# Performance work log

Measured on AMD Instinct MI355X. Metric: run time of the kernel, lower is better.

## Reference

```python
import jax, jax.numpy as jnp
import numpy as np

N_HEADS = 16
N_KV_HEADS = 4
HEAD_DIM = 128
NEG_INF = -1e9


def setup_inputs() -> dict:
    key = jax.random.key(0)
    ks = jax.random.split(key, 6)
    bs, seq, d_model = 2, 2048, 2048
    x = jax.random.normal(ks[0], (bs, seq, d_model), jnp.float32)
    # RoPE table: theta = 10000^{-2i/head_dim}, angle = pos * theta
    inv_freq = 1.0 / (10000.0 ** (jnp.arange(0, HEAD_DIM, 2, dtype=jnp.float32) / HEAD_DIM))
    ang = jnp.arange(seq, dtype=jnp.float32)[:, None] * inv_freq[None, :]  # [seq, head_dim/2]
    freqs_cos = jnp.cos(ang)
    freqs_sin = jnp.sin(ang)
    # causal additive mask
    mask = jnp.where(jnp.tril(jnp.ones((seq, seq), dtype=bool)), 0.0, NEG_INF).astype(jnp.float32)
    s = 1.0 / np.sqrt(d_model)
    wq = jax.random.normal(ks[1], (d_model, N_HEADS * HEAD_DIM), jnp.float32) * s
    wk = jax.random.normal(ks[2], (d_model, N_KV_HEADS * HEAD_DIM), jnp.float32) * s
    wv = jax.random.normal(ks[3], (d_model, N_KV_HEADS * HEAD_DIM), jnp.float32) * s
    wo = jax.random.normal(ks[4], (N_HEADS * HEAD_DIM, d_model), jnp.float32) * s
    return {"x": x, "freqs_cos": freqs_cos, "freqs_sin": freqs_sin, "mask": mask,
            "wq": wq, "wk": wk, "wv": wv, "wo": wo}


def _rope(t, cos, sin):
    # t: [b, h, s, d]; cos/sin: [s, d/2]
    b, h, s, d = t.shape
    tp = t.reshape(b, h, s, d // 2, 2)
    x0, x1 = tp[..., 0], tp[..., 1]
    c = cos[None, None, :, :]
    sn = sin[None, None, :, :]
    o0 = x0 * c - x1 * sn
    o1 = x0 * sn + x1 * c
    return jnp.stack([o0, o1], axis=-1).reshape(b, h, s, d)


def reference(x, freqs_cos, freqs_sin, mask, wq, wk, wv, wo):
    bs, seq, d_model = x.shape
    rep = N_HEADS // N_KV_HEADS
    q = (x @ wq).reshape(bs, seq, N_HEADS, HEAD_DIM).transpose(0, 2, 1, 3)
    k = (x @ wk).reshape(bs, seq, N_KV_HEADS, HEAD_DIM).transpose(0, 2, 1, 3)
    v = (x @ wv).reshape(bs, seq, N_KV_HEADS, HEAD_DIM).transpose(0, 2, 1, 3)
    q = _rope(q, freqs_cos, freqs_sin)
    k = _rope(k, freqs_cos, freqs_sin)
    # GQA: group q heads over kv heads instead of materially repeating kv
    qg = q.reshape(bs, N_KV_HEADS, rep, seq, HEAD_DIM)
    scores = jnp.einsum('bgrsd,bgtd->bgrst', qg, k) / np.sqrt(HEAD_DIM)
    scores = scores + mask[None, None, None, :, :]
    attn = jax.nn.softmax(scores, axis=-1)
    out = jnp.einsum('bgrst,bgtd->bgrsd', attn, v)
    out = out.reshape(bs, N_HEADS, seq, HEAD_DIM).transpose(0, 2, 1, 3).reshape(bs, seq, -1)
    return out @ wo
```

## Files before the change

kernel.cpp:

```cpp
#include <hip/hip_runtime.h>
#include <hip/hip_bf16.h>

#define SEQ 2048
#define DM 2048
#define NH 16
#define NKV 4
#define HD 128

typedef float f32x4 __attribute__((ext_vector_type(4)));
typedef short s16x8 __attribute__((ext_vector_type(8)));
typedef short s16x4 __attribute__((ext_vector_type(4)));

__device__ inline __hip_bfloat16 f2b(float f) { return __float2bfloat16(f); }
__device__ inline float b2f_us(unsigned short u) { return __uint_as_float(((unsigned)u) << 16); }
__device__ inline short f2b_s(float f) {
    __hip_bfloat16 h = __float2bfloat16(f);
    return *(short*)&h;
}

__device__ inline void gl_lds16(const void* g, void* l) {
    __builtin_amdgcn_global_load_lds((const __attribute__((address_space(1))) void*)g,
                                     (__attribute__((address_space(3))) void*)l, 16, 0, 0);
}

__global__ void prep_kernel(const float* __restrict__ x,
                            const float* __restrict__ wq, const float* __restrict__ wk,
                            const float* __restrict__ wv, const float* __restrict__ wo,
                            __hip_bfloat16* __restrict__ xb,
                            __hip_bfloat16* __restrict__ wqkvt,
                            __hip_bfloat16* __restrict__ wot) {
    __shared__ float tile[32][33];
    int bid = blockIdx.x;
    const int t = threadIdx.x;
    if (bid < 8192) {
        int i = (bid * 256 + t) * 4;
        float4 v = *(const float4*)(x + i);
        __hip_bfloat16 o4[4] = {f2b(v.x), f2b(v.y), f2b(v.z), f2b(v.w)};
        *(ushort4*)(xb + i) = *(ushort4*)o4;
        return;
    }
    bid -= 8192;
    const float* in;
    __hip_bfloat16* out;
    int N, bx, by;
    if (bid < 4096) {
        in = wq; out = wqkvt; N = 2048; bx = bid & 63; by = bid >> 6;
    } else if (bid < 5120) {
        bid -= 4096; in = wk; out = wqkvt + (size_t)2048 * 2048; N = 512; bx = bid & 15; by = bid >> 4;
    } else if (bid < 6144) {
        bid -= 5120; in = wv; out = wqkvt + (size_t)2560 * 2048; N = 512; bx = bid & 15; by = bid >> 4;
    } else {
        bid -= 6144; in = wo; out = wot; N = 2048; bx = bid & 63; by = bid >> 6;
    }
    const int K = 2048;
    int n0 = bx * 32, k0 = by * 32;
    int tx = t & 31, ty = t >> 5;
    for (int r = ty; r < 32; r += 8)
        tile[r][tx] = in[(size_t)(k0 + r) * N + n0 + tx];
    __syncthreads();
    for (int r = ty; r < 32; r += 8)
        out[(size_t)(n0 + r) * K + k0 + tx] = f2b(tile[tx][r]);
}

template <int OUT_F32>
__global__ __launch_bounds__(256, 3) void gemm_bt(
    const __hip_bfloat16* __restrict__ A,
    const __hip_bfloat16* __restrict__ Bt,
    void* __restrict__ Cp, int M, int N, int Kd) {
    __shared__ __hip_bfloat16 As[128 * 64];
    __shared__ __hip_bfloat16 Bs[128 * 64];
    const int nx = gridDim.x, ny = gridDim.y;
    const int pid = blockIdx.y * nx + blockIdx.x;
    const int GM = 8;
    const int grp = pid / (GM * nx);
    const int first = grp * GM;
    const int gsz = (ny - first < GM) ? (ny - first) : GM;
    const int mt = first + (pid % gsz);
    const int ntile = (pid % (GM * nx)) / gsz;
    const int m0 = mt * 128, n0 = ntile * 128;

    const int t = threadIdx.x;
    const int wv = t >> 6, lane = t & 63;
    const int wm = (wv >> 1) * 64, wn = (wv & 1) * 64;
    const int lrow = lane & 15, quad = lane >> 4;
    f32x4 acc[4][4];
    f32x4 z4 = {0.f, 0.f, 0.f, 0.f};
    for (int i = 0; i < 4; ++i)
        for (int j = 0; j < 4; ++j) acc[i][j] = z4;

    for (int k0 = 0; k0 < Kd; k0 += 64) {
        __syncthreads();
        for (int i = 0; i < 4; ++i) {
            int flat = i * 256 + t;
            int row = flat >> 3;
            int cb = (flat & 7) ^ (row & 7);
            gl_lds16(A + (size_t)(m0 + row) * Kd + k0 + cb * 8, &As[flat * 8]);
            gl_lds16(Bt + (size_t)(n0 + row) * Kd + k0 + cb * 8, &Bs[flat * 8]);
        }
        __syncthreads();
        for (int kk = 0; kk < 2; ++kk) {
            s16x8 af[4], bf[4];
            for (int i = 0; i < 4; ++i) {
                int ra = wm + i * 16 + lrow;
                int rb = wn + i * 16 + lrow;
                int pba = ((kk * 4 + quad) ^ (ra & 7)) * 8;
                int pbb = ((kk * 4 + quad) ^ (rb & 7)) * 8;
                af[i] = *(const s16x8*)&As[ra * 64 + pba];
                bf[i] = *(const s16x8*)&Bs[rb * 64 + pbb];
            }
            for (int i = 0; i < 4; ++i)
                for (int j = 0; j < 4; ++j)
                    acc[i][j] = __builtin_amdgcn_mfma_f32_16x16x32_bf16(af[i], bf[j],
                                                                        acc[i][j], 0, 0, 0);
        }
    }
    for (int i = 0; i < 4; ++i)
        for (int j = 0; j < 4; ++j)
            for (int r = 0; r < 4; ++r) {
                int m = m0 + wm + i * 16 + quad * 4 + r;
                int n = n0 + wn + j * 16 + lrow;
                if (OUT_F32)
                    ((float*)Cp)[(size_t)m * N + n] = acc[i][j][r];
                else
                    ((__hip_bfloat16*)Cp)[(size_t)m * N + n] = f2b(acc[i][j][r]);
            }
}

#define QSC 0.12751744f
__global__ void rv_kernel(const __hip_bfloat16* __restrict__ qkv,
                          const float* __restrict__ fcos, const float* __restrict__ fsin,
                          __hip_bfloat16* __restrict__ q, __hip_bfloat16* __restrict__ k,
                          __hip_bfloat16* __restrict__ vt) {
    __shared__ __hip_bfloat16 tile[128][136];
    const int t = threadIdx.x;
    if (blockIdx.x < 4096) {
        int tok = blockIdx.x;
        int b = tok >> 11, s = tok & 2047;
        const __hip_bfloat16* row = qkv + (size_t)tok * 3072;
        for (int it = t; it < 320; it += 256) {
            int col = it * 8;
            s16x8 v = *(const s16x8*)(row + col);
            int p0 = (col & 127) >> 1;
            f32x4 c4 = *(const f32x4*)(fcos + s * 64 + p0);
            f32x4 s4 = *(const f32x4*)(fsin + s * 64 + p0);
            float scl = (col < 2048) ? QSC : 1.0f;
            short outv[8];
            for (int p = 0; p < 4; ++p) {
                float x0 = b2f_us((unsigned short)v[2 * p]);
                float x1 = b2f_us((unsigned short)v[2 * p + 1]);
                outv[2 * p] = f2b_s((x0 * c4[p] - x1 * s4[p]) * scl);
                outv[2 * p + 1] = f2b_s((x0 * s4[p] + x1 * c4[p]) * scl);
            }
            int d = col & 127;
            if (col < 2048) {
                int h = col >> 7;
                *(s16x8*)(q + ((size_t)((b * NH + h) * SEQ + s)) * HD + d) = *(s16x8*)outv;
            } else {
                int h = (col - 2048) >> 7;
                *(s16x8*)(k + ((size_t)((b * NKV + h) * SEQ + s)) * HD + d) = *(s16x8*)outv;
            }
        }
        return;
    }
    int r = blockIdx.x - 4096;
    int s0 = (r & 15) * 128;
    int bh = r >> 4;
    int b = bh >> 2, kvh = bh & 3;
    for (int i = 0; i < 8; ++i) {
        int flat = (i * 256 + t) * 8;
        int row = flat >> 7, col = flat & 127;
        *(s16x8*)&tile[row][col] =
            *(const s16x8*)(qkv + (size_t)(b * SEQ + s0 + row) * 3072 + 2560 + kvh * 128 + col);
    }
    __syncthreads();
    for (int i = 0; i < 8; ++i) {
        int dd = i * 16 + (t >> 4);
        int ss = (t & 15) * 8;
        __hip_bfloat16 tmp[8];
        for (int j = 0; j < 8; ++j) tmp[j] = tile[ss + j][dd];
        *(s16x8*)(vt + ((size_t)((b * NKV + kvh) * HD + dd)) * SEQ + s0 + ss) = *(s16x8*)tmp;
    }
}

__global__ __launch_bounds__(512, 4) void attn_kernel(
    const __hip_bfloat16* __restrict__ q, const __hip_bfloat16* __restrict__ k,
    const __hip_bfloat16* __restrict__ vt, __hip_bfloat16* __restrict__ o) {
    __shared__ __hip_bfloat16 Ks[64][136];
    __shared__ __hip_bfloat16 Vs[128][72];

    const int bh = blockIdx.y;
    const int bx = (bh < 16) ? (int)(gridDim.x - 1 - blockIdx.x) : (int)blockIdx.x;
    const int b = bh >> 4, h = bh & 15;
    const int kvh = h >> 2;
    const int t = threadIdx.x;
    const int w = t >> 6, lane = t & 63;
    const int lrow = lane & 15, quad = lane >> 4;
    const int q0 = bx * 128;
    const int qrow = q0 + w * 16 + lrow;

    const __hip_bfloat16* qp = q + ((size_t)((b * NH + h) * SEQ + qrow)) * HD;
    s16x8 qf[4];
    for (int ks = 0; ks < 4; ++ks) qf[ks] = *(const s16x8*)(qp + ks * 32 + quad * 8);

    float m_i = -1e30f, l_i = 0.f;
    f32x4 accO[8];
    f32x4 z4 = {0.f, 0.f, 0.f, 0.f};
    for (int d = 0; d < 8; ++d) accO[d] = z4;

    const __hip_bfloat16* kbase = k + ((size_t)(b * NKV + kvh) * SEQ) * HD;
    const __hip_bfloat16* vbase = vt + ((size_t)(b * NKV + kvh) * HD) * SEQ;

    s16x8 kr[2], vr[2];
    auto load_tile = [&](int kt) {
        for (int i = 0; i < 2; ++i) {
            int flat = (i * 512 + t) * 8;
            kr[i] = *(const s16x8*)(kbase + (size_t)(kt * 64 + (flat >> 7)) * HD + (flat & 127));
            vr[i] = *(const s16x8*)(vbase + (size_t)(flat >> 6) * SEQ + kt * 64 + (flat & 63));
        }
    };
    auto store_tile = [&]() {
        for (int i = 0; i < 2; ++i) {
            int flat = (i * 512 + t) * 8;
            *(s16x8*)&Ks[flat >> 7][flat & 127] = kr[i];
            int row = flat >> 6, k0 = flat & 63;
            int pb = ((k0 >> 5) << 5) | (((k0 >> 2) & 2) << 3) | (((k0 >> 4) & 1) << 2);
            s16x4 lo = {vr[i][0], vr[i][1], vr[i][2], vr[i][3]};
            s16x4 hi = {vr[i][4], vr[i][5], vr[i][6], vr[i][7]};
            *(s16x4*)&Vs[row][pb] = lo;
            *(s16x4*)&Vs[row][pb + 8] = hi;
        }
    };

    const int nkt = 2 * bx + 2;
    load_tile(0);
    store_tile();

    for (int kt = 0; kt < nkt; ++kt) {
        bool more = (kt + 1) < nkt;
        __syncthreads();
        if (more) load_tile(kt + 1);
        bool wave_active = (kt * 64 <= q0 + w * 16 + 15);
        bool mtile = (kt >= 2 * bx);

        if (wave_active) {
            float sv[4][4];
            __builtin_amdgcn_s_setprio(1);
            for (int nt = 0; nt < 4; ++nt) {
                f32x4 sacc = z4;
                for (int ks = 0; ks < 4; ++ks) {
                    s16x8 kf = *(const s16x8*)&Ks[nt * 16 + lrow][ks * 32 + quad * 8];
                    sacc = __builtin_amdgcn_mfma_f32_16x16x32_bf16(kf, qf[ks], sacc, 0, 0, 0);
                }
                if (mtile) {
                    for (int r = 0; r < 4; ++r) {
                        int key = kt * 64 + nt * 16 + quad * 4 + r;
                        sv[nt][r] = (key > qrow) ? -1e30f : sacc[r];
                    }
                } else {
                    for (int r = 0; r < 4; ++r) sv[nt][r] = sacc[r];
                }
            }
            __builtin_amdgcn_s_setprio(0);
            float mt2 = fmaxf(fmaxf(fmaxf(sv[0][0], sv[0][1]), fmaxf(sv[0][2], sv[0][3])),
                              fmaxf(fmaxf(sv[1][0], sv[1][1]), fmaxf(sv[1][2], sv[1][3])));
            mt2 = fmaxf(mt2,
                        fmaxf(fmaxf(fmaxf(sv[2][0], sv[2][1]), fmaxf(sv[2][2], sv[2][3])),
                              fmaxf(fmaxf(sv[3][0], sv[3][1]), fmaxf(sv[3][2], sv[3][3]))));
            mt2 = fmaxf(mt2, __shfl_xor(mt2, 16, 64));
            mt2 = fmaxf(mt2, __shfl_xor(mt2, 32, 64));
            if (!__all(mt2 <= m_i + 8.f)) {
                float mn = fmaxf(m_i, mt2);
                float alpha = exp2f(m_i - mn);
                l_i *= alpha;
                for (int d = 0; d < 8; ++d)
                    for (int r = 0; r < 4; ++r) accO[d][r] *= alpha;
                m_i = mn;
            }
            float rs = 0.f;
            s16x8 pf0, pf1;
#pragma unroll
            for (int j = 0; j < 8; ++j) {
                float p0 = exp2f(sv[j >> 2][j & 3] - m_i);
                float p1 = exp2f(sv[2 + (j >> 2)][j & 3] - m_i);
                rs += p0 + p1;
                pf0[j] = f2b_s(p0);
                pf1[j] = f2b_s(p1);
            }
            rs += __shfl_xor(rs, 16, 64);
            rs += __shfl_xor(rs, 32, 64);
            l_i += rs;
            __builtin_amdgcn_s_setprio(1);
            for (int dt = 0; dt < 8; ++dt) {
                s16x8 vf0 = *(const s16x8*)&Vs[dt * 16 + lrow][quad * 8];
                s16x8 vf1 = *(const s16x8*)&Vs[dt * 16 + lrow][32 + quad * 8];
                accO[dt] = __builtin_amdgcn_mfma_f32_16x16x32_bf16(vf0, pf0, accO[dt], 0, 0, 0);
                accO[dt] = __builtin_amdgcn_mfma_f32_16x16x32_bf16(vf1, pf1, accO[dt], 0, 0, 0);
            }
            __builtin_amdgcn_s_setprio(0);
        }

        __syncthreads();
        if (more) store_tile();
    }
    float inv = 1.0f / l_i;
    __hip_bfloat16* op = o + (size_t)(b * SEQ + qrow) * DM + h * HD;
    for (int dt = 0; dt < 8; ++dt) {
        short ov[4];
        for (int r = 0; r < 4; ++r) ov[r] = f2b_s(accO[dt][r] * inv);
        *(s16x4*)(op + dt * 16 + quad * 4) = *(s16x4*)ov;
    }
}

extern "C" void kernel_launch(void* const* d_in, const int* in_sizes, int n_in,
                              void* d_out, int out_size, void* d_ws, size_t ws_size,
                              hipStream_t stream) {
    (void)in_sizes; (void)n_in; (void)out_size; (void)ws_size;
    const float* x  = (const float*)d_in[0];
    const float* fc = (const float*)d_in[1];
    const float* fs = (const float*)d_in[2];
    const float* wq = (const float*)d_in[4];
    const float* wk = (const float*)d_in[5];
    const float* wv = (const float*)d_in[6];
    const float* wo = (const float*)d_in[7];

    __hip_bfloat16* xb    = (__hip_bfloat16*)d_ws;
    __hip_bfloat16* wqkvt = xb + (size_t)8388608;
    __hip_bfloat16* wot   = wqkvt + (size_t)6291456;
    __hip_bfloat16* qkv   = wot + (size_t)4194304;
    __hip_bfloat16* qb    = xb;
    __hip_bfloat16* kb    = wqkvt;
    __hip_bfloat16* vtb   = wqkvt + (size_t)2097152;
    __hip_bfloat16* attno = qkv;

    prep_kernel<<<18432, 256, 0, stream>>>(x, wq, wk, wv, wo, xb, wqkvt, wot);
    gemm_bt<0><<<dim3(24, 32), 256, 0, stream>>>(xb, wqkvt, qkv, 4096, 3072, 2048);
    rv_kernel<<<4224, 256, 0, stream>>>(qkv, fc, fs, qb, kb, vtb);
    attn_kernel<<<dim3(16, 32), 512, 0, stream>>>(qb, kb, vtb, attno);
    gemm_bt<1><<<dim3(16, 32), 256, 0, stream>>>(attno, wot, d_out, 4096, 2048, 2048);
}
```

Baseline: 331.1 us.

## Switch attention kernel to 32x32x16 MFMA with 4 waves of 32 query rows

Rewrites the attention inner loop to use 32x32x16 bf16 MFMA instead of 16x16x32, with each of 4 waves handling 32 query rows (256 threads per block instead of 512). The P matrix is repacked from the S accumulator layout into B-operand layout using v_permlane32_swap, removing the permuted V store layout in LDS. This is meant to cut LDS reads per FLOP and instruction overhead, but it raises register pressure (larger accumulators, 8 Q fragments) and lowers the wave count per block.

```diff
diff --git a/kernel.cpp b/kernel.cpp
--- a/kernel.cpp
+++ b/kernel.cpp
@@ -8,14 +8,24 @@
 #define HD 128
 
 typedef float f32x4 __attribute__((ext_vector_type(4)));
+typedef float f32x16 __attribute__((ext_vector_type(16)));
 typedef short s16x8 __attribute__((ext_vector_type(8)));
 typedef short s16x4 __attribute__((ext_vector_type(4)));
+typedef unsigned u32x4 __attribute__((ext_vector_type(4)));
 
 __device__ inline __hip_bfloat16 f2b(float f) { return __float2bfloat16(f); }
 __device__ inline float b2f_us(unsigned short u) { return __uint_as_float(((unsigned)u) << 16); }
 __device__ inline short f2b_s(float f) {
     __hip_bfloat16 h = __float2bfloat16(f);
     return *(short*)&h;
+}
+__device__ inline unsigned pk2(float lo, float hi) {
+    unsigned a = (unsigned)(unsigned short)f2b_s(lo);
+    unsigned b = (unsigned)(unsigned short)f2b_s(hi);
+    return a | (b << 16);
+}
+__device__ inline void pl32swap(unsigned& a, unsigned& b) {
+    asm("v_permlane32_swap_b32 %0, %1" : "+v"(a), "+v"(b));
 }
 
 __device__ inline void gl_lds16(const void* g, void* l) {
@@ -182,7 +192,7 @@
     }
 }
 
-__global__ __launch_bounds__(512, 4) void attn_kernel(
+__global__ __launch_bounds__(256, 2) void attn_kernel(
     const __hip_bfloat16* __restrict__ q, const __hip_bfloat16* __restrict__ k,
     const __hip_bfloat16* __restrict__ vt, __hip_bfloat16* __restrict__ o) {
     __shared__ __hip_bfloat16 Ks[64][136];
@@ -190,44 +200,44 @@
 
     const int bh = blockIdx.y;
     const int bx = (bh < 16) ? (int)(gridDim.x - 1 - blockIdx.x) : (int)blockIdx.x;
-    const int b = bh >> 4, h = bh & 15;
-    const int kvh = h >> 2;
+    const int b = bh >> 4, hh = bh & 15;
+    const int kvh = hh >> 2;
     const int t = threadIdx.x;
     const int w = t >> 6, lane = t & 63;
-    const int lrow = lane & 15, quad = lane >> 4;
+    const int l31 = lane & 31, hf = lane >> 5;
     const int q0 = bx * 128;
-    const int qrow = q0 + w * 16 + lrow;
-
-    const __hip_bfloat16* qp = q + ((size_t)((b * NH + h) * SEQ + qrow)) * HD;
-    s16x8 qf[4];
-    for (int ks = 0; ks < 4; ++ks) qf[ks] = *(const s16x8*)(qp + ks * 32 + quad * 8);
+    const int qrow = q0 + w * 32 + l31;
+
+    const __hip_bfloat16* qp = q + ((size_t)((b * NH + hh) * SEQ + qrow)) * HD;
+    s16x8 qf[8];
+#pragma unroll
+    for (int kw = 0; kw < 8; ++kw) qf[kw] = *(const s16x8*)(qp + kw * 16 + hf * 8);
 
     float m_i = -1e30f, l_i = 0.f;
-    f32x4 accO[8];
-    f32x4 z4 = {0.f, 0.f, 0.f, 0.f};
-    for (int d = 0; d < 8; ++d) accO[d] = z4;
+    f32x16 accO[4];
+#pragma unroll
+    for (int db = 0; db < 4; ++db)
+#pragma unroll
+        for (int r = 0; r < 16; ++r) accO[db][r] = 0.f;
 
     const __hip_bfloat16* kbase = k + ((size_t)(b * NKV + kvh) * SEQ) * HD;
     const __hip_bfloat16* vbase = vt + ((size_t)(b * NKV + kvh) * HD) * SEQ;
 
-    s16x8 kr[2], vr[2];
+    s16x8 kr[4], vr[4];
     auto load_tile = [&](int kt) {
-        for (int i = 0; i < 2; ++i) {
-            int flat = (i * 512 + t) * 8;
+#pragma unroll
+        for (int i = 0; i < 4; ++i) {
+            int flat = (i * 256 + t) * 8;
             kr[i] = *(const s16x8*)(kbase + (size_t)(kt * 64 + (flat >> 7)) * HD + (flat & 127));
             vr[i] = *(const s16x8*)(vbase + (size_t)(flat >> 6) * SEQ + kt * 64 + (flat & 63));
         }
     };
     auto store_tile = [&]() {
-        for (int i = 0; i < 2; ++i) {
-            int flat = (i * 512 + t) * 8;
+#pragma unroll
+        for (int i = 0; i < 4; ++i) {
+            int flat = (i * 256 + t) * 8;
             *(s16x8*)&Ks[flat >> 7][flat & 127] = kr[i];
-            int row = flat >> 6, k0 = flat & 63;
-            int pb = ((k0 >> 5) << 5) | (((k0 >> 2) & 2) << 3) | (((k0 >> 4) & 1) << 2);
-            s16x4 lo = {vr[i][0], vr[i][1], vr[i][2], vr[i][3]};
-            s16x4 hi = {vr[i][4], vr[i][5], vr[i][6], vr[i][7]};
-            *(s16x4*)&Vs[row][pb] = lo;
-            *(s16x4*)&Vs[row][pb + 8] = hi;
+            *(s16x8*)&Vs[flat >> 6][flat & 63] = vr[i];
         }
     };
 
@@ -239,62 +249,85 @@
         bool more = (kt + 1) < nkt;
         __syncthreads();
         if (more) load_tile(kt + 1);
-        bool wave_active = (kt * 64 <= q0 + w * 16 + 15);
+        bool wave_active = (kt * 64 <= q0 + w * 32 + 31);
         bool mtile = (kt >= 2 * bx);
 
         if (wave_active) {
-            float sv[4][4];
+            f32x16 s0, s1;
+#pragma unroll
+            for (int r = 0; r < 16; ++r) { s0[r] = 0.f; s1[r] = 0.f; }
             __builtin_amdgcn_s_setprio(1);
-            for (int nt = 0; nt < 4; ++nt) {
-                f32x4 sacc = z4;
-                for (int ks = 0; ks < 4; ++ks) {
-                    s16x8 kf = *(const s16x8*)&Ks[nt * 16 + lrow][ks * 32 + quad * 8];
-                    sacc = __builtin_amdgcn_mfma_f32_16x16x32_bf16(kf, qf[ks], sacc, 0, 0, 0);
+#pragma unroll
+            for (int kw = 0; kw < 8; ++kw) {
+                s16x8 kf0 = *(const s16x8*)&Ks[l31][kw * 16 + hf * 8];
+                s16x8 kf1 = *(const s16x8*)&Ks[32 + l31][kw * 16 + hf * 8];
+                s0 = __builtin_amdgcn_mfma_f32_32x32x16_bf16(kf0, qf[kw], s0, 0, 0, 0);
+                s1 = __builtin_amdgcn_mfma_f32_32x32x16_bf16(kf1, qf[kw], s1, 0, 0, 0);
+            }
+            __builtin_amdgcn_s_setprio(0);
+            if (mtile) {
+#pragma unroll
+                for (int r = 0; r < 16; ++r) {
+                    int key0 = kt * 64 + (r & 3) + 8 * (r >> 2) + 4 * hf;
+                    if (key0 > qrow) s0[r] = -1e30f;
+                    if (key0 + 32 > qrow) s1[r] = -1e30f;
                 }
-                if (mtile) {
-                    for (int r = 0; r < 4; ++r) {
-                        int key = kt * 64 + nt * 16 + quad * 4 + r;
-                        sv[nt][r] = (key > qrow) ? -1e30f : sacc[r];
-                    }
-                } else {
-                    for (int r = 0; r < 4; ++r) sv[nt][r] = sacc[r];
-                }
-            }
-            __builtin_amdgcn_s_setprio(0);
-            float mt2 = fmaxf(fmaxf(fmaxf(sv[0][0], sv[0][1]), fmaxf(sv[0][2], sv[0][3])),
-                              fmaxf(fmaxf(sv[1][0], sv[1][1]), fmaxf(sv[1][2], sv[1][3])));
-            mt2 = fmaxf(mt2,
-                        fmaxf(fmaxf(fmaxf(sv[2][0], sv[2][1]), fmaxf(sv[2][2], sv[2][3])),
-                              fmaxf(fmaxf(sv[3][0], sv[3][1]), fmaxf(sv[3][2], sv[3][3]))));
-            mt2 = fmaxf(mt2, __shfl_xor(mt2, 16, 64));
+            }
+            float mt2 = -1e30f;
+#pragma unroll
+            for (int r = 0; r < 16; ++r) mt2 = fmaxf(mt2, fmaxf(s0[r], s1[r]));
             mt2 = fmaxf(mt2, __shfl_xor(mt2, 32, 64));
             if (!__all(mt2 <= m_i + 8.f)) {
                 float mn = fmaxf(m_i, mt2);
                 float alpha = exp2f(m_i - mn);
                 l_i *= alpha;
-                for (int d = 0; d < 8; ++d)
-                    for (int r = 0; r < 4; ++r) accO[d][r] *= alpha;
+#pragma unroll
+                for (int db = 0; db < 4; ++db)
+#pragma unroll
+                    for (int r = 0; r < 16; ++r) accO[db][r] *= alpha;
                 m_i = mn;
             }
             float rs = 0.f;
-            s16x8 pf0, pf1;
-#pragma unroll
-            for (int j = 0; j < 8; ++j) {
-                float p0 = exp2f(sv[j >> 2][j & 3] - m_i);
-                float p1 = exp2f(sv[2 + (j >> 2)][j & 3] - m_i);
-                rs += p0 + p1;
-                pf0[j] = f2b_s(p0);
-                pf1[j] = f2b_s(p1);
-            }
-            rs += __shfl_xor(rs, 16, 64);
+            unsigned c[16];
+#pragma unroll
+            for (int r = 0; r < 8; ++r) {
+                float pa = exp2f(s0[2 * r] - m_i);
+                float pb = exp2f(s0[2 * r + 1] - m_i);
+                rs += pa + pb;
+                c[r] = pk2(pa, pb);
+            }
+#pragma unroll
+            for (int r = 0; r < 8; ++r) {
+                float pa = exp2f(s1[2 * r] - m_i);
+                float pb = exp2f(s1[2 * r + 1] - m_i);
+                rs += pa + pb;
+                c[8 + r] = pk2(pa, pb);
+            }
             rs += __shfl_xor(rs, 32, 64);
             l_i += rs;
+            pl32swap(c[0], c[2]);  pl32swap(c[1], c[3]);
+            pl32swap(c[4], c[6]);  pl32swap(c[5], c[7]);
+            pl32swap(c[8], c[10]); pl32swap(c[9], c[11]);
+            pl32swap(c[12], c[14]); pl32swap(c[13], c[15]);
+            u32x4 pw0 = {c[0], c[1], c[2], c[3]};
+            u32x4 pw1 = {c[4], c[5], c[6], c[7]};
+            u32x4 pw2 = {c[8], c[9], c[10], c[11]};
+            u32x4 pw3 = {c[12], c[13], c[14], c[15]};
+            s16x8 pf0 = __builtin_bit_cast(s16x8, pw0);
+            s16x8 pf1 = __builtin_bit_cast(s16x8, pw1);
+            s16x8 pf2 = __builtin_bit_cast(s16x8, pw2);
+            s16x8 pf3 = __builtin_bit_cast(s16x8, pw3);
             __builtin_amdgcn_s_setprio(1);
-            for (int dt = 0; dt < 8; ++dt) {
-                s16x8 vf0 = *(const s16x8*)&Vs[dt * 16 + lrow][quad * 8];
-                s16x8 vf1 = *(const s16x8*)&Vs[dt * 16 + lrow][32 + quad * 8];
-                accO[dt] = __builtin_amdgcn_mfma_f32_16x16x32_bf16(vf0, pf0, accO[dt], 0, 0, 0);
-                accO[dt] = __builtin_amdgcn_mfma_f32_16x16x32_bf16(vf1, pf1, accO[dt], 0, 0, 0);
+#pragma unroll
+            for (int db = 0; db < 4; ++db) {
+                s16x8 vf0 = *(const s16x8*)&Vs[db * 32 + l31][0 + hf * 8];
+                s16x8 vf1 = *(const s16x8*)&Vs[db * 32 + l31][16 + hf * 8];
+                s16x8 vf2 = *(const s16x8*)&Vs[db * 32 + l31][32 + hf * 8];
+                s16x8 vf3 = *(const s16x8*)&Vs[db * 32 + l31][48 + hf * 8];
+                accO[db] = __builtin_amdgcn_mfma_f32_32x32x16_bf16(vf0, pf0, accO[db], 0, 0, 0);
+                accO[db] = __builtin_amdgcn_mfma_f32_32x32x16_bf16(vf1, pf1, accO[db], 0, 0, 0);
+                accO[db] = __builtin_amdgcn_mfma_f32_32x32x16_bf16(vf2, pf2, accO[db], 0, 0, 0);
+                accO[db] = __builtin_amdgcn_mfma_f32_32x32x16_bf16(vf3, pf3, accO[db], 0, 0, 0);
             }
             __builtin_amdgcn_s_setprio(0);
         }
@@ -303,12 +336,16 @@
         if (more) store_tile();
     }
     float inv = 1.0f / l_i;
-    __hip_bfloat16* op = o + (size_t)(b * SEQ + qrow) * DM + h * HD;
-    for (int dt = 0; dt < 8; ++dt) {
-        short ov[4];
-        for (int r = 0; r < 4; ++r) ov[r] = f2b_s(accO[dt][r] * inv);
-        *(s16x4*)(op + dt * 16 + quad * 4) = *(s16x4*)ov;
-    }
+    __hip_bfloat16* op = o + (size_t)(b * SEQ + qrow) * DM + hh * HD;
+#pragma unroll
+    for (int db = 0; db < 4; ++db)
+#pragma unroll
+        for (int g = 0; g < 4; ++g) {
+            short ov[4];
+#pragma unroll
+            for (int e = 0; e < 4; ++e) ov[e] = f2b_s(accO[db][4 * g + e] * inv);
+            *(s16x4*)(op + db * 32 + g * 8 + hf * 4) = *(s16x4*)ov;
+        }
 }
 
 extern "C" void kernel_launch(void* const* d_in, const int* in_sizes, int n_in,
@@ -335,6 +372,6 @@
     prep_kernel<<<18432, 256, 0, stream>>>(x, wq, wk, wv, wo, xb, wqkvt, wot);
     gemm_bt<0><<<dim3(24, 32), 256, 0, stream>>>(xb, wqkvt, qkv, 4096, 3072, 2048);
     rv_kernel<<<4224, 256, 0, stream>>>(qkv, fc, fs, qb, kb, vtb);
-    attn_kernel<<<dim3(16, 32), 512, 0, stream>>>(qb, kb, vtb, attno);
+    attn_kernel<<<dim3(16, 32), 256, 0, stream>>>(qb, kb, vtb, attno);
     gemm_bt<1><<<dim3(16, 32), 256, 0, stream>>>(attno, wot, d_out, 4096, 2048, 2048);
 }
```

After: 343.9 us. 1.04x slower.

## Split attention KV range across two wave groups with LDS merge

Applied to the files above, without the earlier changes.

Each block now handles 64 query rows instead of 128, and the grid doubles. The eight waves form two halves that walk disjoint halves of the causal KV range (32-key tiles), each keeping its own online-softmax state. At the end the two partial results are merged through LDS. K tiles are loaded directly into LDS with global_load_lds and an XOR swizzle instead of going through registers. This targets causal load imbalance and the per-block serial KV loop length, at the cost of more blocks, smaller MFMA tiles per step, and an extra merge pass.

```diff
diff --git a/kernel.cpp b/kernel.cpp
--- a/kernel.cpp
+++ b/kernel.cpp
@@ -185,8 +185,12 @@
 __global__ __launch_bounds__(512, 4) void attn_kernel(
     const __hip_bfloat16* __restrict__ q, const __hip_bfloat16* __restrict__ k,
     const __hip_bfloat16* __restrict__ vt, __hip_bfloat16* __restrict__ o) {
-    __shared__ __hip_bfloat16 Ks[64][136];
-    __shared__ __hip_bfloat16 Vs[128][72];
+    __shared__ __attribute__((aligned(16))) char smem[34816];
+    __hip_bfloat16* KsA = (__hip_bfloat16*)smem;
+    __hip_bfloat16* KsB = KsA + 32 * 128;
+    __hip_bfloat16* VsA = KsB + 32 * 128;
+    __hip_bfloat16* VsB = VsA + 128 * 36;
+    float* mrg = (float*)smem;
 
     const int bh = blockIdx.y;
     const int bx = (bh < 16) ? (int)(gridDim.x - 1 - blockIdx.x) : (int)blockIdx.x;
@@ -194,9 +198,11 @@
     const int kvh = h >> 2;
     const int t = threadIdx.x;
     const int w = t >> 6, lane = t & 63;
+    const int g = w & 3, half = w >> 2;
     const int lrow = lane & 15, quad = lane >> 4;
-    const int q0 = bx * 128;
-    const int qrow = q0 + w * 16 + lrow;
+    const int q0 = bx * 64;
+    const int qrow = q0 + g * 16 + lrow;
+    const int Tg = 2 * bx + 1 + (g >> 1);
 
     const __hip_bfloat16* qp = q + ((size_t)((b * NH + h) * SEQ + qrow)) * HD;
     s16x8 qf[4];
@@ -210,50 +216,58 @@
     const __hip_bfloat16* kbase = k + ((size_t)(b * NKV + kvh) * SEQ) * HD;
     const __hip_bfloat16* vbase = vt + ((size_t)(b * NKV + kvh) * HD) * SEQ;
 
-    s16x8 kr[2], vr[2];
-    auto load_tile = [&](int kt) {
-        for (int i = 0; i < 2; ++i) {
-            int flat = (i * 512 + t) * 8;
-            kr[i] = *(const s16x8*)(kbase + (size_t)(kt * 64 + (flat >> 7)) * HD + (flat & 127));
-            vr[i] = *(const s16x8*)(vbase + (size_t)(flat >> 6) * SEQ + kt * 64 + (flat & 63));
-        }
+    auto issue_k = [&](int kt, __hip_bfloat16* dst) {
+        const __hip_bfloat16* src = kbase + (size_t)(kt * 32 + (t >> 4)) * HD +
+                                    (((t & 15) ^ ((t >> 4) & 7)) << 3);
+        gl_lds16(src, dst + t * 8);
     };
-    auto store_tile = [&]() {
-        for (int i = 0; i < 2; ++i) {
-            int flat = (i * 512 + t) * 8;
-            *(s16x8*)&Ks[flat >> 7][flat & 127] = kr[i];
-            int row = flat >> 6, k0 = flat & 63;
-            int pb = ((k0 >> 5) << 5) | (((k0 >> 2) & 2) << 3) | (((k0 >> 4) & 1) << 2);
-            s16x4 lo = {vr[i][0], vr[i][1], vr[i][2], vr[i][3]};
-            s16x4 hi = {vr[i][4], vr[i][5], vr[i][6], vr[i][7]};
-            *(s16x4*)&Vs[row][pb] = lo;
-            *(s16x4*)&Vs[row][pb + 8] = hi;
-        }
+    s16x8 vr[2];
+    auto load_v = [&](int ka, int kb) {
+        int row = t >> 2, k0 = (t & 3) * 8;
+        vr[0] = *(const s16x8*)(vbase + (size_t)row * SEQ + ka * 32 + k0);
+        vr[1] = *(const s16x8*)(vbase + (size_t)row * SEQ + kb * 32 + k0);
     };
-
-    const int nkt = 2 * bx + 2;
-    load_tile(0);
-    store_tile();
-
-    for (int kt = 0; kt < nkt; ++kt) {
-        bool more = (kt + 1) < nkt;
+    auto store_v = [&]() {
+        int row = t >> 2, k0 = (t & 3) * 8;
+        int pb = (((k0 >> 2) & 3) << 3) | (((k0 >> 4) & 1) << 2);
+        s16x4 lo0 = {vr[0][0], vr[0][1], vr[0][2], vr[0][3]};
+        s16x4 hi0 = {vr[0][4], vr[0][5], vr[0][6], vr[0][7]};
+        s16x4 lo1 = {vr[1][0], vr[1][1], vr[1][2], vr[1][3]};
+        s16x4 hi1 = {vr[1][4], vr[1][5], vr[1][6], vr[1][7]};
+        *(s16x4*)&VsA[row * 36 + pb] = lo0;
+        *(s16x4*)&VsA[row * 36 + pb + 8] = hi0;
+        *(s16x4*)&VsB[row * 36 + pb] = lo1;
+        *(s16x4*)&VsB[row * 36 + pb + 8] = hi1;
+    };
+
+    issue_k(0, KsA);
+    issue_k(bx + 1, KsB);
+    load_v(0, bx + 1);
+    store_v();
+
+    for (int s = 0; s <= bx; ++s) {
         __syncthreads();
-        if (more) load_tile(kt + 1);
-        bool wave_active = (kt * 64 <= q0 + w * 16 + 15);
-        bool mtile = (kt >= 2 * bx);
-
-        if (wave_active) {
-            float sv[4][4];
+        const bool more = s < bx;
+        if (more) load_v(s + 1, bx + s + 2);
+
+        const int kt = half ? (bx + 1 + s) : s;
+        const bool active = half ? (bx + 1 + s < Tg) : true;
+        if (active) {
+            const __hip_bfloat16* Ksm = half ? KsB : KsA;
+            const __hip_bfloat16* Vsm = half ? VsB : VsA;
+            const bool mtile = (kt * 32 + 31 > q0 + g * 16);
+            float sv[2][4];
             __builtin_amdgcn_s_setprio(1);
-            for (int nt = 0; nt < 4; ++nt) {
+            for (int nt = 0; nt < 2; ++nt) {
                 f32x4 sacc = z4;
                 for (int ks = 0; ks < 4; ++ks) {
-                    s16x8 kf = *(const s16x8*)&Ks[nt * 16 + lrow][ks * 32 + quad * 8];
+                    s16x8 kf = *(const s16x8*)&Ksm[(nt * 16 + lrow) * 128 +
+                                                   (((ks * 4 + quad) ^ (lrow & 7)) << 3)];
                     sacc = __builtin_amdgcn_mfma_f32_16x16x32_bf16(kf, qf[ks], sacc, 0, 0, 0);
                 }
                 if (mtile) {
                     for (int r = 0; r < 4; ++r) {
-                        int key = kt * 64 + nt * 16 + quad * 4 + r;
+                        int key = kt * 32 + nt * 16 + quad * 4 + r;
                         sv[nt][r] = (key > qrow) ? -1e30f : sacc[r];
                     }
                 } else {
@@ -263,9 +277,6 @@
             __builtin_amdgcn_s_setprio(0);
             float mt2 = fmaxf(fmaxf(fmaxf(sv[0][0], sv[0][1]), fmaxf(sv[0][2], sv[0][3])),
                               fmaxf(fmaxf(sv[1][0], sv[1][1]), fmaxf(sv[1][2], sv[1][3])));
-            mt2 = fmaxf(mt2,
-                        fmaxf(fmaxf(fmaxf(sv[2][0], sv[2][1]), fmaxf(sv[2][2], sv[2][3])),
-                              fmaxf(fmaxf(sv[3][0], sv[3][1]), fmaxf(sv[3][2], sv[3][3]))));
             mt2 = fmaxf(mt2, __shfl_xor(mt2, 16, 64));
             mt2 = fmaxf(mt2, __shfl_xor(mt2, 32, 64));
             if (!__all(mt2 <= m_i + 8.f)) {
@@ -277,37 +288,54 @@
                 m_i = mn;
             }
             float rs = 0.f;
-            s16x8 pf0, pf1;
+            s16x8 pf;
 #pragma unroll
             for (int j = 0; j < 8; ++j) {
-                float p0 = exp2f(sv[j >> 2][j & 3] - m_i);
-                float p1 = exp2f(sv[2 + (j >> 2)][j & 3] - m_i);
-                rs += p0 + p1;
-                pf0[j] = f2b_s(p0);
-                pf1[j] = f2b_s(p1);
+                float p = exp2f(sv[j >> 2][j & 3] - m_i);
+                rs += p;
+                pf[j] = f2b_s(p);
             }
             rs += __shfl_xor(rs, 16, 64);
             rs += __shfl_xor(rs, 32, 64);
             l_i += rs;
             __builtin_amdgcn_s_setprio(1);
             for (int dt = 0; dt < 8; ++dt) {
-                s16x8 vf0 = *(const s16x8*)&Vs[dt * 16 + lrow][quad * 8];
-                s16x8 vf1 = *(const s16x8*)&Vs[dt * 16 + lrow][32 + quad * 8];
-                accO[dt] = __builtin_amdgcn_mfma_f32_16x16x32_bf16(vf0, pf0, accO[dt], 0, 0, 0);
-                accO[dt] = __builtin_amdgcn_mfma_f32_16x16x32_bf16(vf1, pf1, accO[dt], 0, 0, 0);
+                s16x8 vf = *(const s16x8*)&Vsm[(dt * 16 + lrow) * 36 + quad * 8];
+                accO[dt] = __builtin_amdgcn_mfma_f32_16x16x32_bf16(vf, pf, accO[dt], 0, 0, 0);
             }
             __builtin_amdgcn_s_setprio(0);
         }
 
         __syncthreads();
-        if (more) store_tile();
-    }
-    float inv = 1.0f / l_i;
-    __hip_bfloat16* op = o + (size_t)(b * SEQ + qrow) * DM + h * HD;
-    for (int dt = 0; dt < 8; ++dt) {
-        short ov[4];
-        for (int r = 0; r < 4; ++r) ov[r] = f2b_s(accO[dt][r] * inv);
-        *(s16x4*)(op + dt * 16 + quad * 4) = *(s16x4*)ov;
+        if (more) {
+            issue_k(s + 1, KsA);
+            issue_k(bx + s + 2, KsB);
+            store_v();
+        }
+    }
+
+    if (half == 1) {
+        float* p = mrg + (size_t)(g * 64 + lane) * 34;
+        p[0] = m_i;
+        p[1] = l_i;
+        for (int dt = 0; dt < 8; ++dt)
+            for (int r = 0; r < 4; ++r) p[2 + dt * 4 + r] = accO[dt][r];
+    }
+    __syncthreads();
+    if (half == 0) {
+        float* p = mrg + (size_t)(g * 64 + lane) * 34;
+        float mB = p[0], lB = p[1];
+        float mS = fmaxf(m_i, mB);
+        float eA = exp2f(m_i - mS);
+        float eB = exp2f(mB - mS);
+        float inv = 1.0f / (l_i * eA + lB * eB);
+        __hip_bfloat16* op = o + (size_t)(b * SEQ + qrow) * DM + h * HD;
+        for (int dt = 0; dt < 8; ++dt) {
+            short ov[4];
+            for (int r = 0; r < 4; ++r)
+                ov[r] = f2b_s((accO[dt][r] * eA + p[2 + dt * 4 + r] * eB) * inv);
+            *(s16x4*)(op + dt * 16 + quad * 4) = *(s16x4*)ov;
+        }
     }
 }
 
@@ -335,6 +363,6 @@
     prep_kernel<<<18432, 256, 0, stream>>>(x, wq, wk, wv, wo, xb, wqkvt, wot);
     gemm_bt<0><<<dim3(24, 32), 256, 0, stream>>>(xb, wqkvt, qkv, 4096, 3072, 2048);
     rv_kernel<<<4224, 256, 0, stream>>>(qkv, fc, fs, qb, kb, vtb);
-    attn_kernel<<<dim3(16, 32), 512, 0, stream>>>(qb, kb, vtb, attno);
+    attn_kernel<<<dim3(32, 32), 512, 0, stream>>>(qb, kb, vtb, attno);
     gemm_bt<1><<<dim3(16, 32), 256, 0, stream>>>(attno, wot, d_out, 4096, 2048, 2048);
 }
```

New measurement: 523.2 us. +58.0%, slower.
